# Kernel tuning notes

Hardware: AMD Instinct MI355X
Metric: run time of the kernel (lower is better)

## Reference

```python
import jax, jax.numpy as jnp
import numpy as np

W_NBITS = 8
A_NBITS = 8


def _fake_quant_weight_per_channel(w, nbits):
    # symmetric per-output-channel (row) fake quantization
    qmax = float(2 ** (nbits - 1) - 1)
    scale = jnp.max(jnp.abs(w), axis=1, keepdims=True) / qmax  # [out, 1]
    scale = jnp.maximum(scale, 1e-8)
    return jnp.clip(jnp.round(w / scale), -qmax - 1.0, qmax) * scale


def _fake_quant_act_per_group(x, group_size, nbits):
    # dynamic symmetric per-group fake quantization along the feature dim
    qmax = float(2 ** (nbits - 1) - 1)
    tokens, feat = x.shape
    xg = x.reshape(tokens, feat // group_size, group_size)
    scale = jnp.max(jnp.abs(xg), axis=-1, keepdims=True) / qmax  # [T, G, 1]
    scale = jnp.maximum(scale, 1e-8)
    xq = jnp.clip(jnp.round(xg / scale), -qmax - 1.0, qmax) * scale
    return xq.reshape(tokens, feat)


def setup_inputs() -> dict:
    key = jax.random.key(0)
    k1, k2, k3 = jax.random.split(key, 3)
    tokens, in_f, out_f = 8192, 4096, 4096
    x = jax.random.normal(k1, (tokens, in_f), dtype=jnp.float32)
    weight = jax.random.normal(k2, (out_f, in_f), dtype=jnp.float32) * 0.02
    bias = jax.random.normal(k3, (out_f,), dtype=jnp.float32) * 0.02
    return {"x": x, "weight": weight, "bias": bias, "group_size": 128}


def reference(x, weight, bias, group_size):
    w_q = _fake_quant_weight_per_channel(weight, W_NBITS)
    x_q = _fake_quant_act_per_group(x, group_size, A_NBITS)
    # F.linear: x @ w.T + b
    return jnp.einsum("tc,oc->to", x_q, w_q) + bias
```

## Files before the change

kernel.cpp:

```cpp
#include <hip/hip_runtime.h>
#include <stdint.h>


typedef __attribute__((ext_vector_type(4))) int   i32x4;
typedef __attribute__((ext_vector_type(4))) float f32x4;

static __device__ __forceinline__ void load_lds16(const void* g, void* l) {
    __builtin_amdgcn_global_load_lds(
        (const __attribute__((address_space(1))) void*)g,
        (__attribute__((address_space(3))) void*)l, 16, 0, 0);
}

static __device__ __forceinline__ int8_t q8(float v, float scale) {
    float q = rintf(v / scale);
    q = fminf(fmaxf(q, -128.0f), 127.0f);
    return (int8_t)(int)q;
}

__global__ __launch_bounds__(256) void act_quant_kernel(
        const float* __restrict__ x, int8_t* __restrict__ xq,
        float* __restrict__ sxT, int in_f, int M) {
    const int row = blockIdx.x, t = threadIdx.x;
    const float* xr = x + (size_t)row * in_f;
    int8_t* xo = xq + (size_t)row * in_f;
    for (int base = t * 4; base < in_f; base += 256 * 4) {
        float4 v = *(const float4*)(xr + base);
        float m = fmaxf(fmaxf(fabsf(v.x), fabsf(v.y)),
                        fmaxf(fabsf(v.z), fabsf(v.w)));
        m = fmaxf(m, __shfl_xor(m, 1));
        m = fmaxf(m, __shfl_xor(m, 2));
        m = fmaxf(m, __shfl_xor(m, 4));
        m = fmaxf(m, __shfl_xor(m, 8));
        m = fmaxf(m, __shfl_xor(m, 16));
        const float scale = fmaxf(m / 127.0f, 1e-8f);
        char4 o;
        o.x = q8(v.x, scale); o.y = q8(v.y, scale);
        o.z = q8(v.z, scale); o.w = q8(v.w, scale);
        *(char4*)(xo + base) = o;
        if ((t & 31) == 0)
            sxT[(size_t)(base >> 7) * M + row] = scale;
    }
}

__global__ __launch_bounds__(256) void wgt_quant_kernel(
        const float* __restrict__ w, int8_t* __restrict__ wq,
        float* __restrict__ sw, int K) {
    const int row = blockIdx.x, t = threadIdx.x;
    const float* wr = w + (size_t)row * K;
    int8_t* wo = wq + (size_t)row * K;
    float m = 0.0f;
    for (int i = t * 4; i < K; i += 256 * 4) {
        float4 v = *(const float4*)(wr + i);
        m = fmaxf(m, fmaxf(fmaxf(fabsf(v.x), fabsf(v.y)),
                           fmaxf(fabsf(v.z), fabsf(v.w))));
    }
#pragma unroll
    for (int off = 1; off < 64; off <<= 1) m = fmaxf(m, __shfl_xor(m, off));
    __shared__ float wm[4];
    if ((t & 63) == 0) wm[t >> 6] = m;
    __syncthreads();
    m = fmaxf(fmaxf(wm[0], wm[1]), fmaxf(wm[2], wm[3]));
    const float scale = fmaxf(m / 127.0f, 1e-8f);
    if (t == 0) sw[row] = scale;
    for (int i = t * 4; i < K; i += 256 * 4) {
        float4 v = *(const float4*)(wr + i);
        char4 o;
        o.x = q8(v.x, scale); o.y = q8(v.y, scale);
        o.z = q8(v.z, scale); o.w = q8(v.w, scale);
        *(char4*)(wo + i) = o;
    }
}

__global__ __launch_bounds__(256, 2) void gemm_i8_kernel(
        const int8_t* __restrict__ A, const int8_t* __restrict__ B,
        const float* __restrict__ sxT, const float* __restrict__ sw,
        const float* __restrict__ bias, float* __restrict__ C,
        int M, int N, int K) {
    __shared__ __align__(16) int8_t As[128 * 128];
    __shared__ __align__(16) int8_t Bs[128 * 128];
    __shared__ float sxs[128];
    const int tid = threadIdx.x;
    const int wave = tid >> 6, lane = tid & 63;
    const int bm = blockIdx.y * 128, bn = blockIdx.x * 128;
    const int wm = (wave >> 1) * 64, wn = (wave & 1) * 64;

    f32x4 acc[4][4];
#pragma unroll
    for (int i = 0; i < 4; i++)
#pragma unroll
        for (int j = 0; j < 4; j++) acc[i][j] = (f32x4){0.f, 0.f, 0.f, 0.f};

    const int srow = wave * 8 + (lane >> 3);
    const int scol = (((lane & 7) ^ ((lane >> 3) & 7)) * 16);
    const size_t sK = (size_t)K;
    const int8_t* Ag = A + (size_t)(bm + srow) * sK + scol;
    const int8_t* Bg = B + (size_t)(bn + srow) * sK + scol;
    int8_t* AsW = As + (wave * 8) * 128;
    int8_t* BsW = Bs + (wave * 8) * 128;

    const int fr = lane & 15, q = lane >> 4, r7 = lane & 7;
    const int gBase = bm;
    const int G = K >> 7;  (void)G;

    for (int k0 = 0; k0 < K; k0 += 128) {
#pragma unroll
        for (int i = 0; i < 4; i++) {
            load_lds16(Ag + k0 + (size_t)i * 32 * sK, AsW + i * 32 * 128);
            load_lds16(Bg + k0 + (size_t)i * 32 * sK, BsW + i * 32 * 128);
        }
        if (tid < 128) sxs[tid] = sxT[(size_t)(k0 >> 7) * M + gBase + tid];
        __syncthreads();

        i32x4 a[4][2], b[4][2];
        f32x4 sxv[4];
#pragma unroll
        for (int mi = 0; mi < 4; mi++) {
            const int arow = wm + mi * 16 + fr;
            const int brow = wn + mi * 16 + fr;
#pragma unroll
            for (int h = 0; h < 2; h++) {
                a[mi][h] = *(const i32x4*)(As + arow * 128 +
                                           ((h * 4 + q) ^ r7) * 16);
                b[mi][h] = *(const i32x4*)(Bs + brow * 128 +
                                           ((h * 4 + q) ^ r7) * 16);
            }
            sxv[mi] = *(const f32x4*)(sxs + wm + mi * 16 + q * 4);
        }
#pragma unroll
        for (int mi = 0; mi < 4; mi++)
#pragma unroll
            for (int ni = 0; ni < 4; ni++) {
                i32x4 iacc = __builtin_amdgcn_mfma_i32_16x16x64_i8(
                    a[mi][0], b[ni][0], (i32x4){0, 0, 0, 0}, 0, 0, 0);
                iacc = __builtin_amdgcn_mfma_i32_16x16x64_i8(
                    a[mi][1], b[ni][1], iacc, 0, 0, 0);
#pragma unroll
                for (int r = 0; r < 4; r++)
                    acc[mi][ni][r] += (float)iacc[r] * sxv[mi][r];
            }
        __syncthreads();
    }

    const int or0 = bm + wm + q * 4;
    const int oc0 = bn + wn + fr;
    float swv[4], bv[4];
#pragma unroll
    for (int ni = 0; ni < 4; ni++) {
        swv[ni] = sw[oc0 + ni * 16];
        bv[ni] = bias[oc0 + ni * 16];
    }
#pragma unroll
    for (int mi = 0; mi < 4; mi++)
#pragma unroll
        for (int ni = 0; ni < 4; ni++)
#pragma unroll
            for (int r = 0; r < 4; r++)
                C[(size_t)(or0 + mi * 16 + r) * N + (oc0 + ni * 16)] =
                    acc[mi][ni][r] * swv[ni] + bv[ni];
}

extern "C" void kernel_launch(void* const* d_in, const int* in_sizes, int n_in,
                              void* d_out, int out_size, void* d_ws, size_t ws_size,
                              hipStream_t stream) {
    const float* x    = (const float*)d_in[0];
    const float* w    = (const float*)d_in[1];
    const float* bias = (const float*)d_in[2];

    const int out_f  = in_sizes[2];
    const int in_f   = in_sizes[1] / out_f;
    const int tokens = in_sizes[0] / in_f;
    const int G = in_f / 128;

    int8_t* xq  = (int8_t*)d_ws;
    int8_t* wq  = xq + (size_t)tokens * in_f;
    float*  sxT = (float*)(wq + (size_t)out_f * in_f);
    float*  sw  = sxT + (size_t)G * tokens;
    float*  out = (float*)d_out;

    act_quant_kernel<<<tokens, 256, 0, stream>>>(x, xq, sxT, in_f, tokens);
    wgt_quant_kernel<<<out_f, 256, 0, stream>>>(w, wq, sw, in_f);

    dim3 grid(out_f / 128, tokens / 128);
    gemm_i8_kernel<<<grid, 256, 0, stream>>>(xq, wq, sxT, sw, bias, out,
                                             tokens, out_f, in_f);
}
```

Baseline: 454.9 us.

## Fuse activation and weight quant kernels and load act scales directly from global

Merges the activation and weight quantization kernels into one launch, with block index selecting the path. The weight path now keeps the row in registers so weights are read once instead of twice, but it hardcodes K=4096. The GEMM drops its shared-memory staging of activation scales and each lane loads its scale vectors straight from global memory. This is meant to cut launch overhead, redundant weight traffic and one shared-memory round trip.

Measured after the change: 445.1 us. 1.02x faster.

```diff
diff --git a/kernel.cpp b/kernel.cpp
--- a/kernel.cpp
+++ b/kernel.cpp
@@ -17,57 +17,61 @@
     return (int8_t)(int)q;
 }
 
-__global__ __launch_bounds__(256) void act_quant_kernel(
+__global__ __launch_bounds__(256) void quant_fused_kernel(
         const float* __restrict__ x, int8_t* __restrict__ xq,
-        float* __restrict__ sxT, int in_f, int M) {
-    const int row = blockIdx.x, t = threadIdx.x;
-    const float* xr = x + (size_t)row * in_f;
-    int8_t* xo = xq + (size_t)row * in_f;
-    for (int base = t * 4; base < in_f; base += 256 * 4) {
-        float4 v = *(const float4*)(xr + base);
-        float m = fmaxf(fmaxf(fabsf(v.x), fabsf(v.y)),
-                        fmaxf(fabsf(v.z), fabsf(v.w)));
-        m = fmaxf(m, __shfl_xor(m, 1));
-        m = fmaxf(m, __shfl_xor(m, 2));
-        m = fmaxf(m, __shfl_xor(m, 4));
-        m = fmaxf(m, __shfl_xor(m, 8));
-        m = fmaxf(m, __shfl_xor(m, 16));
+        float* __restrict__ sxT,
+        const float* __restrict__ w, int8_t* __restrict__ wq,
+        float* __restrict__ sw, int in_f, int M) {
+    const int b = blockIdx.x, t = threadIdx.x;
+    if (b < M) {
+        const int row = b;
+        const float* xr = x + (size_t)row * in_f;
+        int8_t* xo = xq + (size_t)row * in_f;
+        for (int base = t * 4; base < in_f; base += 256 * 4) {
+            float4 v = *(const float4*)(xr + base);
+            float m = fmaxf(fmaxf(fabsf(v.x), fabsf(v.y)),
+                            fmaxf(fabsf(v.z), fabsf(v.w)));
+            m = fmaxf(m, __shfl_xor(m, 1));
+            m = fmaxf(m, __shfl_xor(m, 2));
+            m = fmaxf(m, __shfl_xor(m, 4));
+            m = fmaxf(m, __shfl_xor(m, 8));
+            m = fmaxf(m, __shfl_xor(m, 16));
+            const float scale = fmaxf(m / 127.0f, 1e-8f);
+            char4 o;
+            o.x = q8(v.x, scale); o.y = q8(v.y, scale);
+            o.z = q8(v.z, scale); o.w = q8(v.w, scale);
+            *(char4*)(xo + base) = o;
+            if ((t & 31) == 0)
+                sxT[(size_t)(base >> 7) * M + row] = scale;
+        }
+    } else {
+        const int row = b - M;
+        const float* wr = w + (size_t)row * in_f;
+        int8_t* wo = wq + (size_t)row * in_f;
+        float4 v[4];
+        float m = 0.0f;
+#pragma unroll
+        for (int i = 0; i < 4; i++) {
+            v[i] = *(const float4*)(wr + t * 4 + i * 1024);
+            m = fmaxf(m, fmaxf(fmaxf(fabsf(v[i].x), fabsf(v[i].y)),
+                               fmaxf(fabsf(v[i].z), fabsf(v[i].w))));
+        }
+#pragma unroll
+        for (int off = 1; off < 64; off <<= 1)
+            m = fmaxf(m, __shfl_xor(m, off));
+        __shared__ float wm[4];
+        if ((t & 63) == 0) wm[t >> 6] = m;
+        __syncthreads();
+        m = fmaxf(fmaxf(wm[0], wm[1]), fmaxf(wm[2], wm[3]));
         const float scale = fmaxf(m / 127.0f, 1e-8f);
-        char4 o;
-        o.x = q8(v.x, scale); o.y = q8(v.y, scale);
-        o.z = q8(v.z, scale); o.w = q8(v.w, scale);
-        *(char4*)(xo + base) = o;
-        if ((t & 31) == 0)
-            sxT[(size_t)(base >> 7) * M + row] = scale;
-    }
-}
-
-__global__ __launch_bounds__(256) void wgt_quant_kernel(
-        const float* __restrict__ w, int8_t* __restrict__ wq,
-        float* __restrict__ sw, int K) {
-    const int row = blockIdx.x, t = threadIdx.x;
-    const float* wr = w + (size_t)row * K;
-    int8_t* wo = wq + (size_t)row * K;
-    float m = 0.0f;
-    for (int i = t * 4; i < K; i += 256 * 4) {
-        float4 v = *(const float4*)(wr + i);
-        m = fmaxf(m, fmaxf(fmaxf(fabsf(v.x), fabsf(v.y)),
-                           fmaxf(fabsf(v.z), fabsf(v.w))));
-    }
+        if (t == 0) sw[row] = scale;
 #pragma unroll
-    for (int off = 1; off < 64; off <<= 1) m = fmaxf(m, __shfl_xor(m, off));
-    __shared__ float wm[4];
-    if ((t & 63) == 0) wm[t >> 6] = m;
-    __syncthreads();
-    m = fmaxf(fmaxf(wm[0], wm[1]), fmaxf(wm[2], wm[3]));
-    const float scale = fmaxf(m / 127.0f, 1e-8f);
-    if (t == 0) sw[row] = scale;
-    for (int i = t * 4; i < K; i += 256 * 4) {
-        float4 v = *(const float4*)(wr + i);
-        char4 o;
-        o.x = q8(v.x, scale); o.y = q8(v.y, scale);
-        o.z = q8(v.z, scale); o.w = q8(v.w, scale);
-        *(char4*)(wo + i) = o;
+        for (int i = 0; i < 4; i++) {
+            char4 o;
+            o.x = q8(v[i].x, scale); o.y = q8(v[i].y, scale);
+            o.z = q8(v[i].z, scale); o.w = q8(v[i].w, scale);
+            *(char4*)(wo + t * 4 + i * 1024) = o;
+        }
     }
 }
 
@@ -78,7 +82,6 @@
         int M, int N, int K) {
     __shared__ __align__(16) int8_t As[128 * 128];
     __shared__ __align__(16) int8_t Bs[128 * 128];
-    __shared__ float sxs[128];
     const int tid = threadIdx.x;
     const int wave = tid >> 6, lane = tid & 63;
     const int bm = blockIdx.y * 128, bn = blockIdx.x * 128;
@@ -99,8 +102,7 @@
     int8_t* BsW = Bs + (wave * 8) * 128;
 
     const int fr = lane & 15, q = lane >> 4, r7 = lane & 7;
-    const int gBase = bm;
-    const int G = K >> 7;  (void)G;
+    const float* sxg = sxT + bm + wm + q * 4;
 
     for (int k0 = 0; k0 < K; k0 += 128) {
 #pragma unroll
@@ -108,11 +110,13 @@
             load_lds16(Ag + k0 + (size_t)i * 32 * sK, AsW + i * 32 * 128);
             load_lds16(Bg + k0 + (size_t)i * 32 * sK, BsW + i * 32 * 128);
         }
-        if (tid < 128) sxs[tid] = sxT[(size_t)(k0 >> 7) * M + gBase + tid];
+        f32x4 sxv[4];
+#pragma unroll
+        for (int mi = 0; mi < 4; mi++)
+            sxv[mi] = *(const f32x4*)(sxg + (size_t)(k0 >> 7) * M + mi * 16);
         __syncthreads();
 
         i32x4 a[4][2], b[4][2];
-        f32x4 sxv[4];
 #pragma unroll
         for (int mi = 0; mi < 4; mi++) {
             const int arow = wm + mi * 16 + fr;
@@ -124,7 +128,6 @@
                 b[mi][h] = *(const i32x4*)(Bs + brow * 128 +
                                            ((h * 4 + q) ^ r7) * 16);
             }
-            sxv[mi] = *(const f32x4*)(sxs + wm + mi * 16 + q * 4);
         }
 #pragma unroll
         for (int mi = 0; mi < 4; mi++)
@@ -177,8 +180,8 @@
     float*  sw  = sxT + (size_t)G * tokens;
     float*  out = (float*)d_out;
 
-    act_quant_kernel<<<tokens, 256, 0, stream>>>(x, xq, sxT, in_f, tokens);
-    wgt_quant_kernel<<<out_f, 256, 0, stream>>>(w, wq, sw, in_f);
+    quant_fused_kernel<<<tokens + out_f, 256, 0, stream>>>(
+        x, xq, sxT, w, wq, sw, in_f, tokens);
 
     dim3 grid(out_f / 128, tokens / 128);
     gemm_i8_kernel<<<grid, 256, 0, stream>>>(xq, wq, sxT, sw, bias, out,
```
